# Performance work log

Measured on AMD Instinct MI355X. Metric: run time of the kernel, lower is better.

Reference implementation:

```python
import jax, jax.numpy as jnp
import numpy as np


def setup_inputs() -> dict:
    key = jax.random.key(0)
    ks = jax.random.split(key, 4)
    B, C, H, W, L = 2, 32, 128, 128, 7
    return {
        "x": jax.random.normal(ks[0], (B, C, H, W), jnp.float32),
        # conv3d3x3: Conv3d(C, 32, (1,3,3)) -> 2D conv weight [32, C, 3, 3]
        "w1": jax.random.normal(ks[1], (32, C, 3, 3), jnp.float32) * 0.05,
        "b1": jnp.zeros((32,), jnp.float32),
        # conv3d1x1: Conv3d(32, 1, 1) -> pointwise weight [1, 32]
        "w2": jax.random.normal(ks[2], (1, 32), jnp.float32) * 0.05,
        "b2": jnp.zeros((1,), jnp.float32),
        # conv3d9x9x1: Conv3d(C, C, (1,L,L)) -> weight [C, C, L, L]
        "w3": jax.random.normal(ks[3], (C, C, L, L), jnp.float32) * 0.02,
        "b3": jnp.zeros((C,), jnp.float32),
        "local_scale": 7,
    }


def reference(x, w1, b1, w2, b2, w3, b3, local_scale):
    # sliding_window branch of Local_attention.forward
    L = int(local_scale)
    pad = L // 2
    B, C, H, W = x.shape
    P = H * W
    # F.unfold with kernel (H, W) and padding=pad over padded input gives the
    # L*L shifted copies of the full feature map. Equivalent gather:
    # local_x[b,c,ki*W+kj,wi,wj] = x_pad[b,c, ki+wi, kj+wj]
    xp = jnp.pad(x, ((0, 0), (0, 0), (pad, pad), (pad, pad)))
    local = jnp.stack(
        [xp[:, :, wi:wi + H, wj:wj + W] for wi in range(L) for wj in range(L)],
        axis=-1,
    )  # [B, C, H, W, L*L]
    local = local.reshape(B, C, P, L, L)
    # Conv3d kernels with depth-size 1 act independently per depth slice ->
    # fold the depth (pixel) dim into the batch and run 2D convs.
    lx = local.transpose(0, 2, 1, 3, 4).reshape(B * P, C, L, L)
    k = jax.lax.conv_general_dilated(
        lx, w1, window_strides=(1, 1), padding=((1, 1), (1, 1)),
        dimension_numbers=("NCHW", "OIHW", "NCHW"),
    ) + b1[None, :, None, None]                      # [B*P, 32, L, L]
    att = jax.nn.sigmoid(
        jnp.einsum("nchw,oc->nohw", k, w2) + b2[None, :, None, None]
    )                                                # [B*P, 1, L, L]
    att_x = lx * att + lx                            # gated residual
    # Conv3d(C, C, (1,L,L)) valid -> full contraction over (C_in, L, L)
    out = jnp.einsum("nchw,ochw->no", att_x, w3) + b3  # [B*P, C]
    output = out.reshape(B, P, C).transpose(0, 2, 1).reshape(B, C, H, W)
    att_mp = att.reshape(B, P, 1, L, L).transpose(0, 2, 1, 3, 4)  # [B,1,P,L,L]
    return output, att_mp
```

## Files before the change

kernel.cpp:

```cpp
#include <hip/hip_runtime.h>
#include <math.h>

typedef __attribute__((ext_vector_type(8))) short bf16x8;
typedef __attribute__((ext_vector_type(4))) float f32x4;
typedef __attribute__((ext_vector_type(4))) unsigned int u32x4;
typedef __attribute__((ext_vector_type(2))) unsigned int u32x2;

namespace {
constexpr int OUT0 = 2 * 32 * 16384;
}

__device__ __forceinline__ unsigned int bf16_rne(float f) {
  unsigned int u = __builtin_bit_cast(unsigned int, f);
  return u + 0x7fffu + ((u >> 16) & 1u);
}
__device__ __forceinline__ unsigned int bf16_rhu(float f) {
  return __builtin_bit_cast(unsigned int, f) + 0x8000u;
}
__device__ __forceinline__ unsigned int pack_rne(float lo, float hi) {
  return __builtin_amdgcn_perm(bf16_rne(hi), bf16_rne(lo), 0x07060302u);
}
__device__ __forceinline__ unsigned int pack_rhu(float lo, float hi) {
  return __builtin_amdgcn_perm(bf16_rhu(hi), bf16_rhu(lo), 0x07060302u);
}
__device__ __forceinline__ float bf16_to_f32(unsigned int u16v) {
  return __builtin_bit_cast(float, u16v << 16);
}

__global__ __launch_bounds__(256) void prep_kernel(
    const float* __restrict__ w1, const float* __restrict__ b1,
    const float* __restrict__ w2, const float* __restrict__ b2,
    const float* __restrict__ w3,
    float* __restrict__ wk, unsigned int* __restrict__ w3f) {
  int t = threadIdx.x, blk = blockIdx.x;
  if (blk < 98) {
    int f = blk * 256 + t;
    int d = f & 3;
    int lane = (f >> 2) & 63;
    int nt = (f >> 8) & 1;
    int ij = f >> 9;
    int o = nt * 16 + (lane & 15);
    int k0 = ((lane >> 4) << 3) + 2 * d;
    float f0 = w3[o * 1568 + k0 * 49 + ij];
    float f1 = w3[o * 1568 + (k0 + 1) * 49 + ij];
    w3f[f] = pack_rne(f0, f1);
  } else {
    int k = (blk - 98) * 256 + t;
    if (k < 288) {
      int c = k / 9, r = k - c * 9;
      float s = 0.f;
#pragma unroll
      for (int o = 0; o < 32; ++o) s += w2[o] * w1[o * 288 + c * 9 + r];
      wk[k] = s;
    } else if (k == 288) {
      float s = b2[0];
#pragma unroll
      for (int o = 0; o < 32; ++o) s += w2[o] * b1[o];
      wk[288] = s;
    }
  }
}

__global__ __launch_bounds__(512, 4) void fused_kernel(
    const float* __restrict__ x, const float* __restrict__ wk,
    const unsigned int* __restrict__ w3f, const float* __restrict__ b3,
    float* __restrict__ out, float* __restrict__ att_out) {
  __shared__ __align__(16) char regA[16384];
  unsigned short* xs16 = (unsigned short*)regA;
  float* as_ = (float*)regA;
  __shared__ __align__(16) unsigned short xh[224 * 40];
  __shared__ unsigned short ysb[9 * 224];
  __shared__ float wks[289];

  int t = threadIdx.x;
  int bi = blockIdx.x;
  int b = bi >> 8;
  int tile = bi & 255;
  int y0 = (tile >> 4) << 3, x0 = (tile & 15) << 3;
  const float* xb = x + ((long)b << 19);

  for (int k = t; k < 289; k += 512) wks[k] = wk[k];

#pragma unroll
  for (int it = 0; it < 4; ++it) {
    int idx = it * 512 + t;
    int c = idx >> 6;
    int r64 = idx & 63;
    int row = r64 >> 2, seg = r64 & 3;
    int gy = y0 + row - 4;
    int gxs = x0 + (seg << 2) - 4;
    f32x4 v = {0.f, 0.f, 0.f, 0.f};
    if ((unsigned)gy < 128u && (unsigned)gxs < 128u)
      v = *reinterpret_cast<const f32x4*>(xb + (c << 14) + (gy << 7) + gxs);
    u32x2 p;
    p[0] = pack_rhu(v[0], v[1]);
    p[1] = pack_rhu(v[2], v[3]);
    *reinterpret_cast<u32x2*>(reinterpret_cast<unsigned int*>(xs16) +
                              (c << 7) + (r64 << 1)) = p;
  }
  __syncthreads();

  if (t < 256) {
    int r = t >> 4;
    bool inner = (unsigned)(r - 1) < 14u;
    int n = t - 16;
    unsigned int u[32];
#pragma unroll
    for (int c = 0; c < 32; ++c) u[c] = xs16[(c << 8) + t];
    float s[9];
#pragma unroll
    for (int dd = 0; dd < 9; ++dd) s[dd] = 0.f;
#pragma unroll
    for (int c = 0; c < 32; ++c) {
      float xf = bf16_to_f32(u[c]);
#pragma unroll
      for (int dd = 0; dd < 9; ++dd) s[dd] += xf * wks[c * 9 + dd];
    }
    if (inner) {
#pragma unroll
      for (int dd = 0; dd < 9; ++dd)
        ysb[dd * 224 + n] = (unsigned short)(bf16_rhu(s[dd]) >> 16);
      unsigned int* xhd = reinterpret_cast<unsigned int*>(xh) + n * 20;
#pragma unroll
      for (int g4 = 0; g4 < 4; ++g4) {
        u32x4 d;
#pragma unroll
        for (int e = 0; e < 4; ++e) {
          int k2 = g4 * 4 + e;
          d[e] = __builtin_amdgcn_perm(u[2 * k2 + 1], u[2 * k2], 0x05040100u);
        }
        *reinterpret_cast<u32x4*>(xhd + g4 * 4) = d;
      }
    }
  }
  __syncthreads();

#pragma unroll 1
  for (int it = 0; it < 7; ++it) {
    int f = it * 512 + t;
    if (f < 3136) {
      int pos = f >> 6;
      int px = f & 63;
      int py = px >> 3, pxl = px & 7;
      int i = pos / 7, j = pos - i * 7;
      float s = wks[288];
#pragma unroll
      for (int di = 0; di < 3; ++di) {
        int ii = i + di - 1;
        if ((unsigned)ii >= 7u) continue;
#pragma unroll
        for (int dj = 0; dj < 3; ++dj) {
          int jj = j + dj - 1;
          if ((unsigned)jj >= 7u) continue;
          s += bf16_to_f32(
              (unsigned int)ysb[(di * 3 + dj) * 224 + (py + ii) * 16 + pxl + jj + 1]);
        }
      }
      as_[pos * 68 + px] = 1.f + 1.f / (1.f + expf(-s));
    }
  }
  __syncthreads();

#pragma unroll 1
  for (int it = 0; it < 7; ++it) {
    int f = it * 512 + t;
    if (f < 3136) {
      int row = f / 392;
      int rem = f - row * 392;
      int pxl = rem / 49;
      int pos = rem - pxl * 49;
      long base = ((long)(b << 14) + ((y0 + row) << 7) + x0) * 49;
      att_out[base + rem] = as_[pos * 68 + (row << 3) + pxl] - 1.f;
    }
  }

  int wv = t >> 6, lane = t & 63;
  int mt = wv >> 1, oh = wv & 1;
  int ml = lane & 15, q = lane >> 4;
  int px = mt * 16 + ml;
  int py = px >> 3, pxl = px & 7;
  f32x4 acc = {0.f, 0.f, 0.f, 0.f};
  const u32x4* bp = reinterpret_cast<const u32x4*>(w3f) + lane + oh * 64;
#pragma unroll 1
  for (int i = 0; i < 7; ++i) {
    int nb = (py + i) * 16 + pxl + 1;
#pragma unroll
    for (int j = 0; j < 7; ++j) {
      int ij = i * 7 + j;
      u32x4 bw = bp[ij * 128];
      bf16x8 af = *reinterpret_cast<const bf16x8*>(&xh[(nb + j) * 40 + (q << 3)]);
      f32x4 gv = *reinterpret_cast<const f32x4*>(&as_[ij * 68 + mt * 16 + (q << 2)]);
      f32x4 z = {0.f, 0.f, 0.f, 0.f};
      f32x4 P = __builtin_amdgcn_mfma_f32_16x16x32_bf16(
          af, __builtin_bit_cast(bf16x8, bw), z, 0, 0, 0);
#pragma unroll
      for (int r = 0; r < 4; ++r) acc[r] += gv[r] * P[r];
    }
  }
  __syncthreads();

  {
    int o = oh * 16 + ml;
    float bv = b3[o];
#pragma unroll
    for (int r = 0; r < 4; ++r)
      as_[o * 68 + mt * 16 + (q << 2) + r] = acc[r] + bv;
  }
  __syncthreads();
#pragma unroll
  for (int rep = 0; rep < 4; ++rep) {
    int idx = rep * 512 + t;
    int o = idx >> 6, pxs = idx & 63;
    out[((long)b << 19) + (o << 14) + ((y0 + (pxs >> 3)) << 7) + x0 + (pxs & 7)]
        = as_[o * 68 + pxs];
  }
}

extern "C" void kernel_launch(void* const* d_in, const int* in_sizes, int n_in,
                              void* d_out, int out_size, void* d_ws, size_t ws_size,
                              hipStream_t stream) {
  const float* x  = (const float*)d_in[0];
  const float* w1 = (const float*)d_in[1];
  const float* b1 = (const float*)d_in[2];
  const float* w2 = (const float*)d_in[3];
  const float* b2 = (const float*)d_in[4];
  const float* w3 = (const float*)d_in[5];
  const float* b3 = (const float*)d_in[6];

  float* out = (float*)d_out;
  float* att_out = out + OUT0;
  float* wk = (float*)d_ws;
  unsigned int* w3f = (unsigned int*)((char*)d_ws + 4096);

  prep_kernel<<<100, 256, 0, stream>>>(w1, b1, w2, b2, w3, wk, w3f);
  fused_kernel<<<512, 512, 0, stream>>>(x, wk, w3f, b3, out, att_out);
}
```

Measured before the change: 89.93 us.

## Split fused kernel into attention kernel and separate global-memory GEMM kernel

Splits the single fused kernel in two. The first computes the attention map, writes it out, and stores a transposed bf16 copy of x plus the gate values to workspace. The second does the gated 7x7 contraction with MFMA, staging the w3 fragments in shared memory and reading x and the gates from global memory with row-strip tiles. This is meant to fix the low occupancy and redundant weight reads of the fused kernel, at the cost of an extra launch and a global-memory round trip for x and the gates.

```diff
diff --git a/kernel.cpp b/kernel.cpp
--- a/kernel.cpp
+++ b/kernel.cpp
@@ -8,6 +8,7 @@
 
 namespace {
 constexpr int OUT0 = 2 * 32 * 16384;
+constexpr int NPIX = 32768;
 }
 
 __device__ __forceinline__ unsigned int bf16_rne(float f) {
@@ -61,14 +62,13 @@
   }
 }
 
-__global__ __launch_bounds__(512, 4) void fused_kernel(
+__global__ __launch_bounds__(256) void att_kernel(
     const float* __restrict__ x, const float* __restrict__ wk,
-    const unsigned int* __restrict__ w3f, const float* __restrict__ b3,
-    float* __restrict__ out, float* __restrict__ att_out) {
+    float* __restrict__ att_out, float* __restrict__ gt,
+    unsigned int* __restrict__ xt) {
   __shared__ __align__(16) char regA[16384];
   unsigned short* xs16 = (unsigned short*)regA;
   float* as_ = (float*)regA;
-  __shared__ __align__(16) unsigned short xh[224 * 40];
   __shared__ unsigned short ysb[9 * 224];
   __shared__ float wks[289];
 
@@ -79,11 +79,11 @@
   int y0 = (tile >> 4) << 3, x0 = (tile & 15) << 3;
   const float* xb = x + ((long)b << 19);
 
-  for (int k = t; k < 289; k += 512) wks[k] = wk[k];
-
-#pragma unroll
-  for (int it = 0; it < 4; ++it) {
-    int idx = it * 512 + t;
+  for (int k = t; k < 289; k += 256) wks[k] = wk[k];
+
+#pragma unroll
+  for (int it = 0; it < 8; ++it) {
+    int idx = it * 256 + t;
     int c = idx >> 6;
     int r64 = idx & 63;
     int row = r64 >> 2, seg = r64 & 3;
@@ -100,10 +100,8 @@
   }
   __syncthreads();
 
-  if (t < 256) {
-    int r = t >> 4;
-    bool inner = (unsigned)(r - 1) < 14u;
-    int n = t - 16;
+  {
+    int r = t >> 4, cc = t & 15;
     unsigned int u[32];
 #pragma unroll
     for (int c = 0; c < 32; ++c) u[c] = xs16[(c << 8) + t];
@@ -116,11 +114,15 @@
 #pragma unroll
       for (int dd = 0; dd < 9; ++dd) s[dd] += xf * wks[c * 9 + dd];
     }
-    if (inner) {
+    if ((unsigned)(r - 1) < 14u) {
+      int n = t - 16;
 #pragma unroll
       for (int dd = 0; dd < 9; ++dd)
         ysb[dd * 224 + n] = (unsigned short)(bf16_rhu(s[dd]) >> 16);
-      unsigned int* xhd = reinterpret_cast<unsigned int*>(xh) + n * 20;
+    }
+    if ((unsigned)(r - 4) < 8u && (unsigned)(cc - 4) < 8u) {
+      int gn = (b << 14) + ((y0 + r - 4) << 7) + (x0 + cc - 4);
+      unsigned int* dst = xt + gn * 16;
 #pragma unroll
       for (int g4 = 0; g4 < 4; ++g4) {
         u32x4 d;
@@ -129,15 +131,15 @@
           int k2 = g4 * 4 + e;
           d[e] = __builtin_amdgcn_perm(u[2 * k2 + 1], u[2 * k2], 0x05040100u);
         }
-        *reinterpret_cast<u32x4*>(xhd + g4 * 4) = d;
+        *reinterpret_cast<u32x4*>(dst + g4 * 4) = d;
       }
     }
   }
   __syncthreads();
 
 #pragma unroll 1
-  for (int it = 0; it < 7; ++it) {
-    int f = it * 512 + t;
+  for (int it = 0; it < 13; ++it) {
+    int f = it * 256 + t;
     if (f < 3136) {
       int pos = f >> 6;
       int px = f & 63;
@@ -162,57 +164,84 @@
   __syncthreads();
 
 #pragma unroll 1
-  for (int it = 0; it < 7; ++it) {
-    int f = it * 512 + t;
+  for (int it = 0; it < 13; ++it) {
+    int f = it * 256 + t;
     if (f < 3136) {
       int row = f / 392;
       int rem = f - row * 392;
-      int pxl = rem / 49;
-      int pos = rem - pxl * 49;
+      int pxl2 = rem / 49;
+      int pos2 = rem - pxl2 * 49;
       long base = ((long)(b << 14) + ((y0 + row) << 7) + x0) * 49;
-      att_out[base + rem] = as_[pos * 68 + (row << 3) + pxl] - 1.f;
+      att_out[base + rem] = as_[pos2 * 68 + (row << 3) + pxl2] - 1.f;
+
+      int pos = f >> 6, px = f & 63;
+      int py = px >> 3, pxl = px & 7;
+      gt[pos * NPIX + (b << 14) + ((y0 + py) << 7) + x0 + pxl] = as_[pos * 68 + px];
+    }
+  }
+}
+
+__global__ __launch_bounds__(256) void gemm_kernel(
+    const unsigned int* __restrict__ xt, const float* __restrict__ gt,
+    const unsigned int* __restrict__ w3f, const float* __restrict__ b3,
+    float* __restrict__ out) {
+  __shared__ __align__(16) unsigned int bL[12544];
+
+  int t = threadIdx.x;
+  int oh = blockIdx.x & 1, bm = blockIdx.x >> 1;
+
+#pragma unroll 1
+  for (int it = 0; it < 13; ++it) {
+    int k = it * 256 + t;
+    if (k < 3136) {
+      int ij = k >> 6, ln = k & 63;
+      u32x4 v = *reinterpret_cast<const u32x4*>(w3f + ((ij * 128 + oh * 64 + ln) << 2));
+      *reinterpret_cast<u32x4*>(bL + (k << 2)) = v;
     }
   }
 
   int wv = t >> 6, lane = t & 63;
-  int mt = wv >> 1, oh = wv & 1;
   int ml = lane & 15, q = lane >> 4;
-  int px = mt * 16 + ml;
-  int py = px >> 3, pxl = px & 7;
+  int n0 = bm * 64 + wv * 16;
+  int b = n0 >> 14;
+  int p0 = n0 & 16383;
+  int h0 = p0 >> 7, w0 = p0 & 127;
+  float b3v = b3[oh * 16 + ml];
   f32x4 acc = {0.f, 0.f, 0.f, 0.f};
-  const u32x4* bp = reinterpret_cast<const u32x4*>(w3f) + lane + oh * 64;
+  __syncthreads();
+
 #pragma unroll 1
   for (int i = 0; i < 7; ++i) {
-    int nb = (py + i) * 16 + pxl + 1;
+    int hh = h0 + i - 3;
+    if ((unsigned)hh >= 128u) continue;
+    int nrow = (b << 14) + (hh << 7);
 #pragma unroll
     for (int j = 0; j < 7; ++j) {
       int ij = i * 7 + j;
-      u32x4 bw = bp[ij * 128];
-      bf16x8 af = *reinterpret_cast<const bf16x8*>(&xh[(nb + j) * 40 + (q << 3)]);
-      f32x4 gv = *reinterpret_cast<const f32x4*>(&as_[ij * 68 + mt * 16 + (q << 2)]);
+      int wl = w0 + ml + j - 3;
+      bool okw = (unsigned)wl < 128u;
+      int nn = okw ? (nrow + wl) : n0;
+      u32x4 bw = *reinterpret_cast<const u32x4*>(bL + ((ij * 64 + lane) << 2));
+      u32x4 araw = *reinterpret_cast<const u32x4*>(xt + nn * 16 + (q << 2));
+      if (!okw) { araw[0] = 0; araw[1] = 0; araw[2] = 0; araw[3] = 0; }
+      f32x4 gv = *reinterpret_cast<const f32x4*>(gt + ij * NPIX + n0 + (q << 2));
       f32x4 z = {0.f, 0.f, 0.f, 0.f};
       f32x4 P = __builtin_amdgcn_mfma_f32_16x16x32_bf16(
-          af, __builtin_bit_cast(bf16x8, bw), z, 0, 0, 0);
+          __builtin_bit_cast(bf16x8, araw), __builtin_bit_cast(bf16x8, bw), z, 0, 0, 0);
 #pragma unroll
       for (int r = 0; r < 4; ++r) acc[r] += gv[r] * P[r];
     }
   }
-  __syncthreads();
-
-  {
-    int o = oh * 16 + ml;
-    float bv = b3[o];
-#pragma unroll
-    for (int r = 0; r < 4; ++r)
-      as_[o * 68 + mt * 16 + (q << 2) + r] = acc[r] + bv;
-  }
-  __syncthreads();
-#pragma unroll
-  for (int rep = 0; rep < 4; ++rep) {
-    int idx = rep * 512 + t;
-    int o = idx >> 6, pxs = idx & 63;
-    out[((long)b << 19) + (o << 14) + ((y0 + (pxs >> 3)) << 7) + x0 + (pxs & 7)]
-        = as_[o * 68 + pxs];
+
+  __syncthreads();
+  float* sc = reinterpret_cast<float*>(bL) + wv * 272;
+#pragma unroll
+  for (int r = 0; r < 4; ++r)
+    sc[ml * 17 + (q << 2) + r] = acc[r] + b3v;
+#pragma unroll
+  for (int pp = 0; pp < 4; ++pp) {
+    int od = (pp << 2) + q;
+    out[((long)b << 19) + ((oh * 16 + od) << 14) + p0 + ml] = sc[od * 17 + ml];
   }
 }
 
@@ -229,9 +258,14 @@
 
   float* out = (float*)d_out;
   float* att_out = out + OUT0;
-  float* wk = (float*)d_ws;
-  unsigned int* w3f = (unsigned int*)((char*)d_ws + 4096);
+
+  char* ws = (char*)d_ws;
+  float* wk = (float*)ws;
+  unsigned int* w3f = (unsigned int*)(ws + 4096);
+  unsigned int* xt  = (unsigned int*)(ws + 131072);
+  float* gt = (float*)(ws + 131072 + 2097152);
 
   prep_kernel<<<100, 256, 0, stream>>>(w1, b1, w2, b2, w3, wk, w3f);
-  fused_kernel<<<512, 512, 0, stream>>>(x, wk, w3f, b3, out, att_out);
-}
+  att_kernel<<<512, 256, 0, stream>>>(x, wk, att_out, gt, xt);
+  gemm_kernel<<<1024, 256, 0, stream>>>(xt, gt, w3f, b3, out);
+}
```

Result: slower. 119.8 us (+33.3%).

## Split output-channel halves across blocks and store MFMA results directly

Applied to the files above, without the earlier changes.

Each 8x8 tile is now handled by two 256-thread blocks, one per half of the output channels, giving 1024 blocks instead of 512 blocks of 512 threads. The halo load, the attention-map computation and the sigmoid are duplicated in both blocks, and only one of them writes att_out. The final LDS transpose and its two barriers are replaced by direct float4 global stores from the MFMA accumulators. The sigmoid now uses the hardware exp2 and reciprocal builtins. The split is meant to raise the number of blocks in flight, at the cost of loading x and computing the attention map twice per tile.

```diff
diff --git a/kernel.cpp b/kernel.cpp
--- a/kernel.cpp
+++ b/kernel.cpp
@@ -61,7 +61,7 @@
   }
 }
 
-__global__ __launch_bounds__(512, 4) void fused_kernel(
+__global__ __launch_bounds__(256, 4) void fused_kernel(
     const float* __restrict__ x, const float* __restrict__ wk,
     const unsigned int* __restrict__ w3f, const float* __restrict__ b3,
     float* __restrict__ out, float* __restrict__ att_out) {
@@ -74,16 +74,18 @@
 
   int t = threadIdx.x;
   int bi = blockIdx.x;
-  int b = bi >> 8;
-  int tile = bi & 255;
+  int oh = bi & 1;
+  int tb = bi >> 1;
+  int b = tb >> 8;
+  int tile = tb & 255;
   int y0 = (tile >> 4) << 3, x0 = (tile & 15) << 3;
   const float* xb = x + ((long)b << 19);
 
-  for (int k = t; k < 289; k += 512) wks[k] = wk[k];
-
-#pragma unroll
-  for (int it = 0; it < 4; ++it) {
-    int idx = it * 512 + t;
+  for (int k = t; k < 289; k += 256) wks[k] = wk[k];
+
+#pragma unroll
+  for (int it = 0; it < 8; ++it) {
+    int idx = it * 256 + t;
     int c = idx >> 6;
     int r64 = idx & 63;
     int row = r64 >> 2, seg = r64 & 3;
@@ -100,7 +102,7 @@
   }
   __syncthreads();
 
-  if (t < 256) {
+  {
     int r = t >> 4;
     bool inner = (unsigned)(r - 1) < 14u;
     int n = t - 16;
@@ -136,8 +138,8 @@
   __syncthreads();
 
 #pragma unroll 1
-  for (int it = 0; it < 7; ++it) {
-    int f = it * 512 + t;
+  for (int it = 0; it < 13; ++it) {
+    int f = it * 256 + t;
     if (f < 3136) {
       int pos = f >> 6;
       int px = f & 63;
@@ -156,31 +158,33 @@
               (unsigned int)ysb[(di * 3 + dj) * 224 + (py + ii) * 16 + pxl + jj + 1]);
         }
       }
-      as_[pos * 68 + px] = 1.f + 1.f / (1.f + expf(-s));
+      float e = __builtin_amdgcn_exp2f(s * -1.44269504088896f);
+      as_[pos * 68 + px] = 1.f + __builtin_amdgcn_rcpf(1.f + e);
     }
   }
   __syncthreads();
 
+  if (oh == 0) {
 #pragma unroll 1
-  for (int it = 0; it < 7; ++it) {
-    int f = it * 512 + t;
-    if (f < 3136) {
-      int row = f / 392;
-      int rem = f - row * 392;
-      int pxl = rem / 49;
-      int pos = rem - pxl * 49;
-      long base = ((long)(b << 14) + ((y0 + row) << 7) + x0) * 49;
-      att_out[base + rem] = as_[pos * 68 + (row << 3) + pxl] - 1.f;
+    for (int it = 0; it < 13; ++it) {
+      int f = it * 256 + t;
+      if (f < 3136) {
+        int row = f / 392;
+        int rem = f - row * 392;
+        int pxl = rem / 49;
+        int pos = rem - pxl * 49;
+        long base = ((long)(b << 14) + ((y0 + row) << 7) + x0) * 49;
+        att_out[base + rem] = as_[pos * 68 + (row << 3) + pxl] - 1.f;
+      }
     }
   }
 
   int wv = t >> 6, lane = t & 63;
-  int mt = wv >> 1, oh = wv & 1;
   int ml = lane & 15, q = lane >> 4;
-  int px = mt * 16 + ml;
+  int px = wv * 16 + ml;
   int py = px >> 3, pxl = px & 7;
   f32x4 acc = {0.f, 0.f, 0.f, 0.f};
-  const u32x4* bp = reinterpret_cast<const u32x4*>(w3f) + lane + oh * 64;
+  const u32x4* bp = reinterpret_cast<const u32x4*>(w3f) + oh * 64 + lane;
 #pragma unroll 1
   for (int i = 0; i < 7; ++i) {
     int nb = (py + i) * 16 + pxl + 1;
@@ -189,7 +193,7 @@
       int ij = i * 7 + j;
       u32x4 bw = bp[ij * 128];
       bf16x8 af = *reinterpret_cast<const bf16x8*>(&xh[(nb + j) * 40 + (q << 3)]);
-      f32x4 gv = *reinterpret_cast<const f32x4*>(&as_[ij * 68 + mt * 16 + (q << 2)]);
+      f32x4 gv = *reinterpret_cast<const f32x4*>(&as_[ij * 68 + wv * 16 + (q << 2)]);
       f32x4 z = {0.f, 0.f, 0.f, 0.f};
       f32x4 P = __builtin_amdgcn_mfma_f32_16x16x32_bf16(
           af, __builtin_bit_cast(bf16x8, bw), z, 0, 0, 0);
@@ -197,22 +201,17 @@
       for (int r = 0; r < 4; ++r) acc[r] += gv[r] * P[r];
     }
   }
-  __syncthreads();
 
   {
-    int o = oh * 16 + ml;
-    float bv = b3[o];
-#pragma unroll
-    for (int r = 0; r < 4; ++r)
-      as_[o * 68 + mt * 16 + (q << 2) + r] = acc[r] + bv;
-  }
-  __syncthreads();
-#pragma unroll
-  for (int rep = 0; rep < 4; ++rep) {
-    int idx = rep * 512 + t;
-    int o = idx >> 6, pxs = idx & 63;
-    out[((long)b << 19) + (o << 14) + ((y0 + (pxs >> 3)) << 7) + x0 + (pxs & 7)]
-        = as_[o * 68 + pxs];
+    float bv = b3[(oh << 4) + ml];
+    f32x4 res;
+#pragma unroll
+    for (int r = 0; r < 4; ++r) res[r] = acc[r] + bv;
+    int pyd = (wv << 1) + (q >> 1);
+    int pxd = (q & 1) << 2;
+    float* dst = out + ((long)b << 19) + (((oh << 4) + ml) << 14) +
+                 ((y0 + pyd) << 7) + x0 + pxd;
+    *reinterpret_cast<f32x4*>(dst) = res;
   }
 }
 
@@ -233,5 +232,5 @@
   unsigned int* w3f = (unsigned int*)((char*)d_ws + 4096);
 
   prep_kernel<<<100, 256, 0, stream>>>(w1, b1, w2, b2, w3, wk, w3f);
-  fused_kernel<<<512, 512, 0, stream>>>(x, wk, w3f, b3, out, att_out);
-}
+  fused_kernel<<<1024, 256, 0, stream>>>(x, wk, w3f, b3, out, att_out);
+}
```

Result: slower. 98.82 us (+9.9%).

## Specialize warps: half store attention output while half run MFMA contraction

Applied to the files above, without the earlier changes.

Splits the block so waves 4-7 write the attention map to global memory while waves 0-3 run the MFMA contraction, each of those waves computing both output-channel halves for its pixel tile with two accumulators. Results are written straight from registers as float4 stores, which drops the shared-memory staging and two barriers. The sigmoid switches to hardware exp2 and reciprocal intrinsics. The intent is to overlap the large att_out store traffic with the matrix work, at the cost of halving the number of waves doing MFMA and slightly less precise sigmoid arithmetic.

```diff
diff --git a/kernel.cpp b/kernel.cpp
--- a/kernel.cpp
+++ b/kernel.cpp
@@ -156,63 +156,64 @@
               (unsigned int)ysb[(di * 3 + dj) * 224 + (py + ii) * 16 + pxl + jj + 1]);
         }
       }
-      as_[pos * 68 + px] = 1.f + 1.f / (1.f + expf(-s));
+      float e = __builtin_amdgcn_exp2f(s * -1.44269504088896f);
+      as_[pos * 68 + px] = 1.f + __builtin_amdgcn_rcpf(1.f + e);
     }
   }
   __syncthreads();
 
+  int wv = t >> 6, lane = t & 63;
+  if (wv >= 4) {
+    int tt = t - 256;
 #pragma unroll 1
-  for (int it = 0; it < 7; ++it) {
-    int f = it * 512 + t;
-    if (f < 3136) {
-      int row = f / 392;
-      int rem = f - row * 392;
-      int pxl = rem / 49;
-      int pos = rem - pxl * 49;
-      long base = ((long)(b << 14) + ((y0 + row) << 7) + x0) * 49;
-      att_out[base + rem] = as_[pos * 68 + (row << 3) + pxl] - 1.f;
-    }
-  }
-
-  int wv = t >> 6, lane = t & 63;
-  int mt = wv >> 1, oh = wv & 1;
-  int ml = lane & 15, q = lane >> 4;
-  int px = mt * 16 + ml;
-  int py = px >> 3, pxl = px & 7;
-  f32x4 acc = {0.f, 0.f, 0.f, 0.f};
-  const u32x4* bp = reinterpret_cast<const u32x4*>(w3f) + lane + oh * 64;
+    for (int it = 0; it < 13; ++it) {
+      int f = it * 256 + tt;
+      if (f < 3136) {
+        int row = f / 392;
+        int rem = f - row * 392;
+        int pxl = rem / 49;
+        int pos = rem - pxl * 49;
+        long base = ((long)(b << 14) + ((y0 + row) << 7) + x0) * 49;
+        att_out[base + rem] = as_[pos * 68 + (row << 3) + pxl] - 1.f;
+      }
+    }
+  } else {
+    int ml = lane & 15, q = lane >> 4;
+    int px = (wv << 4) + ml;
+    int py = px >> 3, pxl = px & 7;
+    f32x4 acc0 = {0.f, 0.f, 0.f, 0.f}, acc1 = {0.f, 0.f, 0.f, 0.f};
+    const u32x4* bp = reinterpret_cast<const u32x4*>(w3f) + lane;
 #pragma unroll 1
-  for (int i = 0; i < 7; ++i) {
-    int nb = (py + i) * 16 + pxl + 1;
-#pragma unroll
-    for (int j = 0; j < 7; ++j) {
-      int ij = i * 7 + j;
-      u32x4 bw = bp[ij * 128];
-      bf16x8 af = *reinterpret_cast<const bf16x8*>(&xh[(nb + j) * 40 + (q << 3)]);
-      f32x4 gv = *reinterpret_cast<const f32x4*>(&as_[ij * 68 + mt * 16 + (q << 2)]);
-      f32x4 z = {0.f, 0.f, 0.f, 0.f};
-      f32x4 P = __builtin_amdgcn_mfma_f32_16x16x32_bf16(
-          af, __builtin_bit_cast(bf16x8, bw), z, 0, 0, 0);
-#pragma unroll
-      for (int r = 0; r < 4; ++r) acc[r] += gv[r] * P[r];
-    }
-  }
-  __syncthreads();
-
-  {
-    int o = oh * 16 + ml;
-    float bv = b3[o];
-#pragma unroll
-    for (int r = 0; r < 4; ++r)
-      as_[o * 68 + mt * 16 + (q << 2) + r] = acc[r] + bv;
-  }
-  __syncthreads();
-#pragma unroll
-  for (int rep = 0; rep < 4; ++rep) {
-    int idx = rep * 512 + t;
-    int o = idx >> 6, pxs = idx & 63;
-    out[((long)b << 19) + (o << 14) + ((y0 + (pxs >> 3)) << 7) + x0 + (pxs & 7)]
-        = as_[o * 68 + pxs];
+    for (int i = 0; i < 7; ++i) {
+      int nb = (py + i) * 16 + pxl + 1;
+#pragma unroll
+      for (int j = 0; j < 7; ++j) {
+        int ij = i * 7 + j;
+        u32x4 bw0 = bp[ij * 128];
+        u32x4 bw1 = bp[ij * 128 + 64];
+        bf16x8 af = *reinterpret_cast<const bf16x8*>(&xh[(nb + j) * 40 + (q << 3)]);
+        f32x4 gv = *reinterpret_cast<const f32x4*>(&as_[ij * 68 + (wv << 4) + (q << 2)]);
+        f32x4 z = {0.f, 0.f, 0.f, 0.f};
+        f32x4 P0 = __builtin_amdgcn_mfma_f32_16x16x32_bf16(
+            af, __builtin_bit_cast(bf16x8, bw0), z, 0, 0, 0);
+        f32x4 P1 = __builtin_amdgcn_mfma_f32_16x16x32_bf16(
+            af, __builtin_bit_cast(bf16x8, bw1), z, 0, 0, 0);
+#pragma unroll
+        for (int r = 0; r < 4; ++r) {
+          acc0[r] += gv[r] * P0[r];
+          acc1[r] += gv[r] * P1[r];
+        }
+      }
+    }
+    float bv0 = b3[ml], bv1 = b3[16 + ml];
+    f32x4 r0, r1;
+#pragma unroll
+    for (int r = 0; r < 4; ++r) { r0[r] = acc0[r] + bv0; r1[r] = acc1[r] + bv1; }
+    int pyd = (wv << 1) + (q >> 1);
+    int pxd = (q & 1) << 2;
+    float* dst = out + ((long)b << 19) + ((y0 + pyd) << 7) + x0 + pxd;
+    *reinterpret_cast<f32x4*>(dst + (ml << 14)) = r0;
+    *reinterpret_cast<f32x4*>(dst + ((16 + ml) << 14)) = r1;
   }
 }
 
```

New measurement: 90.85 us. No clear change (+1.0%).
